# Optimization experiments

Hardware: AMD Instinct MI355X
Metric: run time of the kernel (lower is better)

Reference implementation:

```python
import jax, jax.numpy as jnp
import numpy as np

NUM_HEADS = 12
DIM = 768
HEAD_DIM = DIM // NUM_HEADS
NUM_BUCKETS = 32
MAX_DISTANCE = 128
ELEV_SCALE = 1000.0


def _bucket_positions(relative_position):
    # Faithful port of RelativePositionBias2D._bucket_positions (torch .long() truncates;
    # values passed through the large branch are non-negative so astype(int32) matches).
    nb = NUM_BUCKETS // 2  # 16
    n = -relative_position
    ret = (n < 0).astype(jnp.int32) * nb
    n = jnp.abs(n)
    max_exact = nb // 2  # 8
    is_small = n < max_exact
    n_safe = jnp.maximum(n, 1).astype(jnp.float32)  # avoid log(0); masked by is_small
    val_if_large = max_exact + (
        jnp.log(n_safe / max_exact) / np.float32(np.log(MAX_DISTANCE / max_exact)) * (nb - max_exact)
    ).astype(jnp.int32)
    val_if_large = jnp.minimum(val_if_large, nb - 1)
    return ret + jnp.where(is_small, n, val_if_large)


def _bucket_idx(coords_2d):
    # coords_2d: [B, N, 2] in [0,1] -> integer grid coords
    coords_int = (coords_2d * MAX_DISTANCE).astype(jnp.int32)
    rel_x = coords_int[:, :, None, 0] - coords_int[:, None, :, 0]  # [B,N,N]
    rel_y = coords_int[:, :, None, 1] - coords_int[:, None, :, 1]
    bx = _bucket_positions(rel_x)
    by = _bucket_positions(rel_y)
    return bx * NUM_BUCKETS + by  # [B,N,N] int32 in [0, 1024)


def setup_inputs() -> dict:
    key = jax.random.key(0)
    ks = jax.random.split(key, 8)
    B, N, D = 4, 1024, DIM
    x = jax.random.normal(ks[0], (B, N, D), dtype=jnp.float32)
    coords_2d = jax.random.uniform(ks[1], (B, N, 2), dtype=jnp.float32)
    elevation_patches = jax.random.normal(ks[2], (B, N), dtype=jnp.float32) * 2000.0  # meters
    qkv_w = jax.random.normal(ks[3], (3 * D, D), dtype=jnp.float32) * 0.02
    qkv_b = jnp.zeros((3 * D,), dtype=jnp.float32)
    proj_w = jax.random.normal(ks[4], (D, D), dtype=jnp.float32) * 0.02
    proj_b = jnp.zeros((D,), dtype=jnp.float32)
    bias_table = jax.random.normal(ks[5], (NUM_BUCKETS * NUM_BUCKETS, NUM_HEADS), dtype=jnp.float32) * 0.02
    alpha = jnp.full((1,), 2.0, dtype=jnp.float32)
    return {"x": x, "coords_2d": coords_2d, "elevation_patches": elevation_patches,
            "qkv_w": qkv_w, "qkv_b": qkv_b, "proj_w": proj_w, "proj_b": proj_b,
            "bias_table": bias_table, "alpha": alpha}


def reference(x, coords_2d, elevation_patches, qkv_w, qkv_b, proj_w, proj_b, bias_table, alpha):
    B, N, D = x.shape
    H, hd = NUM_HEADS, HEAD_DIM
    scale = hd ** -0.5

    qkv = x @ qkv_w.T + qkv_b  # [B,N,3D]
    qkv = qkv.reshape(B, N, 3, H, hd)
    q = qkv[:, :, 0].transpose(0, 2, 1, 3)  # [B,H,N,hd]
    k = qkv[:, :, 1].transpose(0, 2, 1, 3)
    v = qkv[:, :, 2].transpose(0, 2, 1, 3)

    attn = jnp.einsum('bhnd,bhmd->bhnm', q * scale, k)  # [B,H,N,N]

    # relative position bias: gather from table, [B,N,N,H] -> [B,H,N,N]
    idx = _bucket_idx(coords_2d)
    rel_bias = bias_table[idx].transpose(0, 3, 1, 2)
    attn = attn + rel_bias

    # elevation bias: [B,N,N], broadcast over heads
    elev_diff = (elevation_patches[:, None, :] - elevation_patches[:, :, None]) / ELEV_SCALE
    elev_bias = jnp.clip(-alpha[0] * jax.nn.relu(elev_diff), -10.0, 0.0)
    attn = attn + elev_bias[:, None, :, :]

    attn = jax.nn.softmax(attn.astype(jnp.float32), axis=-1).astype(q.dtype)

    out = jnp.einsum('bhnm,bhmd->bhnd', attn, v)  # [B,H,N,hd]
    out = out.transpose(0, 2, 1, 3).reshape(B, N, D)
    return out @ proj_w.T + proj_b
```

## Files before the change

### kernel.cpp

```cpp
#include <hip/hip_runtime.h>
#include <hip/hip_bf16.h>
#include <math.h>

#define NH 12
#define HD 64
#define NSEQ 1024
#define DMODEL 768
#define LOG2E 1.44269504f

typedef unsigned short ushort_t;
typedef float f32x4 __attribute__((ext_vector_type(4)));
typedef short bf16x8 __attribute__((ext_vector_type(8)));

__device__ __forceinline__ ushort_t f2bf(float f) {
    unsigned int u = __float_as_uint(f);
    u += 0x7FFFu + ((u >> 16) & 1u);
    return (ushort_t)(u >> 16);
}

__device__ __forceinline__ unsigned pk2(float x, float y) {
    __hip_bfloat162 t = __float22bfloat162_rn(make_float2(x, y));
    union { __hip_bfloat162 b; unsigned u; } c; c.b = t;
    return c.u;
}

__device__ __forceinline__ void gl_lds16(const ushort_t* g, ushort_t* l) {
    __builtin_amdgcn_global_load_lds(
        (const __attribute__((address_space(1))) unsigned int*)g,
        (__attribute__((address_space(3))) unsigned int*)l, 16, 0, 0);
}

#define XB_N   3145728u
#define WQB_N  1769472u
#define PWB_N  589824u
#define CVT_BLOCKS 2688

__device__ __forceinline__ int bucketf(int rel) {
    const int n = -rel;
    const int u = (n < 0) ? 16 : 0;
    const int a = n < 0 ? -n : n;
    if (a < 8) return u + a;
    int v = 8 + (int)(log2f((float)a * 0.125f) * 2.0f + 1e-4f);
    if (v > 15) v = 15;
    return u + v;
}

__global__ __launch_bounds__(256) void prep_kernel(
    const float* __restrict__ x, const float* __restrict__ w1,
    const float* __restrict__ w2, ushort_t* __restrict__ dst,
    const float* __restrict__ coords, const float* __restrict__ elev,
    const float* __restrict__ alpha_p, unsigned* __restrict__ pack)
{
    const int t = threadIdx.x;
    if (blockIdx.x < CVT_BLOCKS) {
        const unsigned i = blockIdx.x * 256 + t;
        const unsigned n0 = XB_N / 8, n1 = n0 + WQB_N / 8, n2 = n1 + PWB_N / 8;
        if (i >= n2) return;
        const float* src; unsigned off;
        if (i < n0)      { src = x;  off = i; }
        else if (i < n1) { src = w1; off = i - n0; }
        else             { src = w2; off = i - n1; }
        const float4 a = ((const float4*)src)[off * 2];
        const float4 b = ((const float4*)src)[off * 2 + 1];
        uint4 pk;
        pk.x = pk2(a.x, a.y); pk.y = pk2(a.z, a.w);
        pk.z = pk2(b.x, b.y); pk.w = pk2(b.z, b.w);
        ((uint4*)dst)[i] = pk;
    } else {
        const int blk = blockIdx.x - CVT_BLOCKS;
        const int b = blk >> 10, i = blk & 1023;
        const float alpha = alpha_p[0];
        const float2 ci = *(const float2*)&coords[(size_t)(b * NSEQ + i) * 2];
        const int cxi = (int)(ci.x * 128.0f), cyi = (int)(ci.y * 128.0f);
        const float ei = elev[b * NSEQ + i];
        const int j0 = t * 4;
        const float4 c01 = *(const float4*)&coords[(size_t)(b * NSEQ + j0) * 2];
        const float4 c23 = *(const float4*)&coords[(size_t)(b * NSEQ + j0 + 2) * 2];
        const float4 ej4 = *(const float4*)&elev[b * NSEQ + j0];
        const float cjx[4] = {c01.x, c01.z, c23.x, c23.z};
        const float cjy[4] = {c01.y, c01.w, c23.y, c23.w};
        const float ejv[4] = {ej4.x, ej4.y, ej4.z, ej4.w};
        unsigned r[4];
        #pragma unroll
        for (int k = 0; k < 4; ++k) {
            const int bx = bucketf(cxi - (int)(cjx[k] * 128.0f));
            const int by = bucketf(cyi - (int)(cjy[k] * 128.0f));
            const int idx = (bx << 5) + by;
            const float ed = (ejv[k] - ei) * 1e-3f;
            const float eb = fmaxf(-alpha * fmaxf(ed, 0.0f), -10.0f) * LOG2E;
            r[k] = ((unsigned)f2bf(eb) << 16) | (unsigned)idx;
        }
        uint4 o; o.x = r[0]; o.y = r[1]; o.z = r[2]; o.w = r[3];
        *(uint4*)&pack[((size_t)b << 20) + (size_t)i * NSEQ + j0] = o;
    }
}

__global__ __launch_bounds__(256) void qkv_gemm(
    const ushort_t* __restrict__ A, const ushort_t* __restrict__ B,
    const float* __restrict__ bias,
    ushort_t* __restrict__ Qb, ushort_t* __restrict__ Kb, ushort_t* __restrict__ Vtb)
{
    __shared__ __align__(16) ushort_t SM[6144];
    ushort_t* Asb = SM;
    ushort_t* Bsb = SM + 4096;
    const int t = threadIdx.x;
    const int lane = t & 63, w = t >> 6;
    const int wr = w >> 1, wc = w & 1;
    const int col = lane & 15, quad = lane >> 4;
    const int m0 = blockIdx.y * 128, c0 = blockIdx.x * 64;

    const f32x4 zero = {0.f, 0.f, 0.f, 0.f};
    f32x4 acc[4][2];
    #pragma unroll
    for (int i = 0; i < 4; ++i)
        #pragma unroll
        for (int j = 0; j < 2; ++j) acc[i][j] = zero;

    const int arow = w * 32 + (lane >> 2);
    const int brow = w * 16 + (lane >> 2);
    const int scol = (lane & 3) * 8;
    const ushort_t* Ag = A + (size_t)(m0 + arow) * DMODEL + scol;
    const ushort_t* Bg = B + (size_t)(c0 + brow) * DMODEL + scol;
    ushort_t* Asw = Asb + w * 32 * 32;
    ushort_t* Bsw = Bsb + w * 16 * 32;

    for (int k0 = 0; k0 < DMODEL; k0 += 32) {
        __syncthreads();
        gl_lds16(Ag + k0, Asw);
        gl_lds16(Ag + (size_t)16 * DMODEL + k0, Asw + 16 * 32);
        gl_lds16(Bg + k0, Bsw);
        __syncthreads();
        bf16x8 af[4], bf[2];
        #pragma unroll
        for (int im = 0; im < 4; ++im)
            af[im] = *(const bf16x8*)&Asb[(wr * 64 + im * 16 + col) * 32 + quad * 8];
        #pragma unroll
        for (int jn = 0; jn < 2; ++jn)
            bf[jn] = *(const bf16x8*)&Bsb[(wc * 32 + jn * 16 + col) * 32 + quad * 8];
        #pragma unroll
        for (int im = 0; im < 4; ++im)
            #pragma unroll
            for (int jn = 0; jn < 2; ++jn)
                acc[im][jn] = __builtin_amdgcn_mfma_f32_16x16x32_bf16(af[im], bf[jn], acc[im][jn], 0, 0, 0);
    }

    const int s = c0 / DMODEL;
    const int h = (c0 % DMODEL) >> 6;
    const int b = m0 >> 10;
    const int bh = b * NH + h;
    const int n0 = (m0 & (NSEQ - 1)) + wr * 64;
    const int d0 = (c0 & 63);
    const int cb = c0 + wc * 32;

    __syncthreads();

    if (s < 2) {
        ushort_t* lt = SM + w * 1280;
        ushort_t* dst = (s == 0) ? Qb : Kb;
        const float sc = (s == 0) ? 0.125f * LOG2E : 1.0f;
        float bv[2];
        #pragma unroll
        for (int jn = 0; jn < 2; ++jn) bv[jn] = bias[cb + jn * 16 + col];
        const int row16 = lane >> 2, seg = lane & 3;
        #pragma unroll
        for (int im = 0; im < 4; ++im) {
            #pragma unroll
            for (int jn = 0; jn < 2; ++jn) {
                const f32x4 a = acc[im][jn];
                #pragma unroll
                for (int r = 0; r < 4; ++r)
                    lt[(quad * 4 + r) * 40 + jn * 16 + col] = f2bf((a[r] + bv[jn]) * sc);
            }
            const uint4 u0 = *(const uint4*)&lt[row16 * 40 + seg * 8];
            const size_t gb = ((size_t)bh * NSEQ + n0 + im * 16 + row16) * HD
                            + wc * 32 + seg * 8;
            *(uint4*)&dst[gb] = u0;
        }
    } else {
        #pragma unroll
        for (int im = 0; im < 4; ++im) {
            #pragma unroll
            for (int jn = 0; jn < 2; ++jn) {
                const int d = wc * 32 + jn * 16 + col;
                const float bvv = bias[cb + jn * 16 + col];
                const f32x4 a = acc[im][jn];
                uint2 p;
                p.x = pk2(a[0] + bvv, a[1] + bvv);
                p.y = pk2(a[2] + bvv, a[3] + bvv);
                *(uint2*)&Vtb[((size_t)bh * HD + d) * NSEQ + n0 + im * 16 + quad * 4] = p;
            }
        }
    }
    (void)d0;
}

__global__ __launch_bounds__(256) void attn_mfma(
    const ushort_t* __restrict__ Qb, const ushort_t* __restrict__ Kb,
    const ushort_t* __restrict__ Vtb,
    const unsigned* __restrict__ pack,
    const float* __restrict__ table,
    ushort_t* __restrict__ Ob)
{
    __shared__ __align__(16) ushort_t Ks[2][64 * 72];
    __shared__ __align__(16) ushort_t Vt[2][64 * 72];
    __shared__ __align__(16) ushort_t Ps[64 * 72];
    __shared__ ushort_t tabu[1024];

    const int t = threadIdx.x;
    const int lane = t & 63, w = t >> 6;
    const int col = lane & 15, quad = lane >> 4;
    const int bid = blockIdx.x;
    const int it = bid & 15, bh = bid >> 4;
    const int h = bh % NH, b = bh / NH;
    const int i0 = it * 64;

    for (int i = t; i < 1024; i += 256)
        tabu[i] = f2bf(table[i * NH + h] * LOG2E);

    const ushort_t* Qg = Qb + ((size_t)bh * NSEQ + i0 + w * 16 + col) * HD;
    const bf16x8 aq0 = *(const bf16x8*)(Qg + quad * 8);
    const bf16x8 aq1 = *(const bf16x8*)(Qg + 32 + quad * 8);

    const size_t kvbase = (size_t)bh * NSEQ * HD;
    const unsigned* prow = pack + ((size_t)b << 20)
                         + (size_t)(i0 + w * 16 + col) * NSEQ + quad * 4;

    const int srow = t >> 3, sc8 = (t & 7) * 8;
    const int so0 = srow * 72 + sc8;
    const int so1 = (srow + 32) * 72 + sc8;

    uint4 k0 = *(const uint4*)&Kb[kvbase + (size_t)srow * HD + sc8];
    uint4 k1 = *(const uint4*)&Kb[kvbase + (size_t)(srow + 32) * HD + sc8];
    uint4 v0 = *(const uint4*)&Vtb[kvbase + (size_t)srow * NSEQ + sc8];
    uint4 v1 = *(const uint4*)&Vtb[kvbase + (size_t)(srow + 32) * NSEQ + sc8];
    *(uint4*)&Ks[0][so0] = k0;
    *(uint4*)&Ks[0][so1] = k1;
    *(uint4*)&Vt[0][so0] = v0;
    *(uint4*)&Vt[0][so1] = v1;
    k0 = *(const uint4*)&Kb[kvbase + (size_t)(64 + srow) * HD + sc8];
    k1 = *(const uint4*)&Kb[kvbase + (size_t)(64 + srow + 32) * HD + sc8];
    v0 = *(const uint4*)&Vtb[kvbase + (size_t)srow * NSEQ + 64 + sc8];
    v1 = *(const uint4*)&Vtb[kvbase + (size_t)(srow + 32) * NSEQ + 64 + sc8];

    const f32x4 zero = {0.f, 0.f, 0.f, 0.f};
    f32x4 o_acc[4];
    #pragma unroll
    for (int i = 0; i < 4; ++i) o_acc[i] = zero;
    float l_l = 0.f;

    #pragma unroll 2
    for (int jt = 0; jt < 16; ++jt) {
        __syncthreads();
        const int cur = jt & 1;
        const int j0 = jt * 64;

        if (jt < 15) {
            *(uint4*)&Ks[cur ^ 1][so0] = k0;
            *(uint4*)&Ks[cur ^ 1][so1] = k1;
            *(uint4*)&Vt[cur ^ 1][so0] = v0;
            *(uint4*)&Vt[cur ^ 1][so1] = v1;
        }
        if (jt < 14) {
            const int j2 = (jt + 2) * 64;
            k0 = *(const uint4*)&Kb[kvbase + (size_t)(j2 + srow) * HD + sc8];
            k1 = *(const uint4*)&Kb[kvbase + (size_t)(j2 + srow + 32) * HD + sc8];
            v0 = *(const uint4*)&Vtb[kvbase + (size_t)srow * NSEQ + j2 + sc8];
            v1 = *(const uint4*)&Vtb[kvbase + (size_t)(srow + 32) * NSEQ + j2 + sc8];
        }
        uint4 pk4[4];
        #pragma unroll
        for (int jb = 0; jb < 4; ++jb)
            pk4[jb] = *(const uint4*)(prow + j0 + jb * 16);

        f32x4 sacc[4];
        #pragma unroll
        for (int jb = 0; jb < 4; ++jb) {
            sacc[jb] = zero;
            const bf16x8 kb0 = *(const bf16x8*)&Ks[cur][(jb * 16 + col) * 72 + quad * 8];
            const bf16x8 kb1 = *(const bf16x8*)&Ks[cur][(jb * 16 + col) * 72 + 32 + quad * 8];
            sacc[jb] = __builtin_amdgcn_mfma_f32_16x16x32_bf16(kb0, aq0, sacc[jb], 0, 0, 0);
            sacc[jb] = __builtin_amdgcn_mfma_f32_16x16x32_bf16(kb1, aq1, sacc[jb], 0, 0, 0);
        }

        float rbeb[4][4];
        #pragma unroll
        for (int jb = 0; jb < 4; ++jb) {
            const uint4 pkv = pk4[jb];
            rbeb[jb][0] = __uint_as_float((unsigned)tabu[pkv.x & 1023u] << 16) + __uint_as_float(pkv.x & 0xFFFF0000u);
            rbeb[jb][1] = __uint_as_float((unsigned)tabu[pkv.y & 1023u] << 16) + __uint_as_float(pkv.y & 0xFFFF0000u);
            rbeb[jb][2] = __uint_as_float((unsigned)tabu[pkv.z & 1023u] << 16) + __uint_as_float(pkv.z & 0xFFFF0000u);
            rbeb[jb][3] = __uint_as_float((unsigned)tabu[pkv.w & 1023u] << 16) + __uint_as_float(pkv.w & 0xFFFF0000u);
        }

        float psum = 0.f;
        #pragma unroll
        for (int jb = 0; jb < 4; ++jb) {
            const float p0 = exp2f(sacc[jb][0] + rbeb[jb][0]);
            const float p1 = exp2f(sacc[jb][1] + rbeb[jb][1]);
            const float p2 = exp2f(sacc[jb][2] + rbeb[jb][2]);
            const float p3 = exp2f(sacc[jb][3] + rbeb[jb][3]);
            psum += (p0 + p1) + (p2 + p3);
            uint2 st;
            st.x = pk2(p0, p1);
            st.y = pk2(p2, p3);
            *(uint2*)&Ps[(w * 16 + col) * 72 + jb * 16 + quad * 4] = st;
        }
        l_l += psum;

        const bf16x8 ap0 = *(const bf16x8*)&Ps[(w * 16 + col) * 72 + quad * 8];
        const bf16x8 ap1 = *(const bf16x8*)&Ps[(w * 16 + col) * 72 + 32 + quad * 8];
        #pragma unroll
        for (int db = 0; db < 4; ++db) {
            const bf16x8 vv0 = *(const bf16x8*)&Vt[cur][(db * 16 + col) * 72 + quad * 8];
            const bf16x8 vv1 = *(const bf16x8*)&Vt[cur][(db * 16 + col) * 72 + 32 + quad * 8];
            o_acc[db] = __builtin_amdgcn_mfma_f32_16x16x32_bf16(ap0, vv0, o_acc[db], 0, 0, 0);
            o_acc[db] = __builtin_amdgcn_mfma_f32_16x16x32_bf16(ap1, vv1, o_acc[db], 0, 0, 0);
        }
    }

    float l = l_l;
    l += __shfl_xor(l, 16);
    l += __shfl_xor(l, 32);
    #pragma unroll
    for (int r = 0; r < 4; ++r) {
        const float lr = __shfl(l, w * 16 + quad * 4 + r);
        const float inv = 1.f / lr;
        const int ri = w * 16 + quad * 4 + r;
        const size_t base = ((size_t)(b * NSEQ) + i0 + ri) * DMODEL + h * HD;
        #pragma unroll
        for (int db = 0; db < 4; ++db)
            Ob[base + db * 16 + col] = f2bf(o_acc[db][r] * inv);
    }
}

__global__ __launch_bounds__(256) void proj_gemm(
    const ushort_t* __restrict__ A, const ushort_t* __restrict__ B,
    const float* __restrict__ bias, float* __restrict__ out)
{
    __shared__ __align__(16) ushort_t As[64 * 32];
    __shared__ __align__(16) ushort_t Bs[64 * 32];
    const int t = threadIdx.x;
    const int lane = t & 63, w = t >> 6;
    const int wr = w >> 1, wc = w & 1;
    const int col = lane & 15, quad = lane >> 4;
    const int m0 = blockIdx.y * 64, c0 = blockIdx.x * 64;

    const f32x4 zero = {0.f, 0.f, 0.f, 0.f};
    f32x4 acc[2][2];
    #pragma unroll
    for (int i = 0; i < 2; ++i)
        #pragma unroll
        for (int j = 0; j < 2; ++j) acc[i][j] = zero;

    const int srow = w * 16 + (lane >> 2);
    const int scol = (lane & 3) * 8;
    const ushort_t* Ag = A + (size_t)(m0 + srow) * DMODEL + scol;
    const ushort_t* Bg = B + (size_t)(c0 + srow) * DMODEL + scol;
    ushort_t* Asw = &As[w * 16 * 32];
    ushort_t* Bsw = &Bs[w * 16 * 32];

    for (int k0 = 0; k0 < DMODEL; k0 += 32) {
        __syncthreads();
        gl_lds16(Ag + k0, Asw);
        gl_lds16(Bg + k0, Bsw);
        __syncthreads();
        bf16x8 af[2], bf[2];
        #pragma unroll
        for (int im = 0; im < 2; ++im)
            af[im] = *(const bf16x8*)&As[(wr * 32 + im * 16 + col) * 32 + quad * 8];
        #pragma unroll
        for (int jn = 0; jn < 2; ++jn)
            bf[jn] = *(const bf16x8*)&Bs[(wc * 32 + jn * 16 + col) * 32 + quad * 8];
        #pragma unroll
        for (int im = 0; im < 2; ++im)
            #pragma unroll
            for (int jn = 0; jn < 2; ++jn)
                acc[im][jn] = __builtin_amdgcn_mfma_f32_16x16x32_bf16(af[im], bf[jn], acc[im][jn], 0, 0, 0);
    }

    #pragma unroll
    for (int im = 0; im < 2; ++im) {
        #pragma unroll
        for (int jn = 0; jn < 2; ++jn) {
            const int c = c0 + wc * 32 + jn * 16 + col;
            const float bv = bias[c];
            #pragma unroll
            for (int r = 0; r < 4; ++r) {
                const int m = m0 + wr * 32 + im * 16 + quad * 4 + r;
                out[(size_t)m * DMODEL + c] = acc[im][jn][r] + bv;
            }
        }
    }
}

extern "C" void kernel_launch(void* const* d_in, const int* in_sizes, int n_in,
                              void* d_out, int out_size, void* d_ws, size_t ws_size,
                              hipStream_t stream) {
    const float* x       = (const float*)d_in[0];
    const float* coords  = (const float*)d_in[1];
    const float* elev    = (const float*)d_in[2];
    const float* qkv_w   = (const float*)d_in[3];
    const float* qkv_b   = (const float*)d_in[4];
    const float* proj_w  = (const float*)d_in[5];
    const float* proj_b  = (const float*)d_in[6];
    const float* btable  = (const float*)d_in[7];
    const float* alpha   = (const float*)d_in[8];
    float* out = (float*)d_out;

    ushort_t* wsu = (ushort_t*)d_ws;
    ushort_t* xb  = wsu;
    ushort_t* wqb = wsu + 3145728;
    ushort_t* pwb = wsu + 4915200;
    ushort_t* Qb  = wsu + 5505024;
    ushort_t* Kb  = wsu + 8650752;
    ushort_t* Vtb = wsu + 11796480;
    ushort_t* Ob  = wsu + 14942208;
    unsigned* pck = (unsigned*)(wsu + 18087936);

    prep_kernel<<<CVT_BLOCKS + 4096, 256, 0, stream>>>(
        x, qkv_w, proj_w, wsu, coords, elev, alpha, pck);
    qkv_gemm<<<dim3(36, 32), 256, 0, stream>>>(xb, wqb, qkv_b, Qb, Kb, Vtb);
    attn_mfma<<<768, 256, 0, stream>>>(Qb, Kb, Vtb, pck, btable, Ob);
    proj_gemm<<<dim3(12, 64), 256, 0, stream>>>(Ob, pwb, proj_b, out);
}
```

Measured before the change: 186.4 us.

## Software-pipeline bias pack loads and remap block order in attention kernel

Prefetches the packed relative-position/elevation bias words two tiles ahead and computes each next tile's bias lookups while the P·V MFMAs run, so the global-load latency and LDS table lookups overlap with matrix work. It also remaps blockIdx so consecutive blocks fall on different (batch, head) groups, which should spread work across XCDs and improve K/V cache locality. The MFMA sections are wrapped in s_setprio to favour matrix issue. In exchange it raises register pressure (extra bias and pack arrays) and adds a barrier before the first table use.

After: 185.9 us. Within noise of the previous version (-0.2%).

```diff
diff --git a/kernel.cpp b/kernel.cpp
--- a/kernel.cpp
+++ b/kernel.cpp
@@ -194,6 +194,9 @@
     (void)d0;
 }
 
+#define RBIAS(u) (__uint_as_float((unsigned)tabu[(u) & 1023u] << 16) \
+                + __uint_as_float((u) & 0xFFFF0000u))
+
 __global__ __launch_bounds__(256) void attn_mfma(
     const ushort_t* __restrict__ Qb, const ushort_t* __restrict__ Kb,
     const ushort_t* __restrict__ Vtb,
@@ -209,7 +212,7 @@
     const int t = threadIdx.x;
     const int lane = t & 63, w = t >> 6;
     const int col = lane & 15, quad = lane >> 4;
-    const int bid = blockIdx.x;
+    const int bid = (blockIdx.x & 7) * 96 + (blockIdx.x >> 3);
     const int it = bid & 15, bh = bid >> 4;
     const int h = bh % NH, b = bh / NH;
     const int i0 = it * 64;
@@ -242,6 +245,26 @@
     v0 = *(const uint4*)&Vtb[kvbase + (size_t)srow * NSEQ + 64 + sc8];
     v1 = *(const uint4*)&Vtb[kvbase + (size_t)(srow + 32) * NSEQ + 64 + sc8];
 
+    uint4 pk4g[4], pk4l[4];
+    #pragma unroll
+    for (int jb = 0; jb < 4; ++jb)
+        pk4g[jb] = *(const uint4*)(prow + jb * 16);
+
+    __syncthreads();
+
+    float rbc[4][4], rbn[4][4];
+    #pragma unroll
+    for (int jb = 0; jb < 4; ++jb) {
+        const uint4 pkv = pk4g[jb];
+        rbc[jb][0] = RBIAS(pkv.x);
+        rbc[jb][1] = RBIAS(pkv.y);
+        rbc[jb][2] = RBIAS(pkv.z);
+        rbc[jb][3] = RBIAS(pkv.w);
+    }
+    #pragma unroll
+    for (int jb = 0; jb < 4; ++jb)
+        pk4g[jb] = *(const uint4*)(prow + 64 + jb * 16);
+
     const f32x4 zero = {0.f, 0.f, 0.f, 0.f};
     f32x4 o_acc[4];
     #pragma unroll
@@ -252,7 +275,6 @@
     for (int jt = 0; jt < 16; ++jt) {
         __syncthreads();
         const int cur = jt & 1;
-        const int j0 = jt * 64;
 
         if (jt < 15) {
             *(uint4*)&Ks[cur ^ 1][so0] = k0;
@@ -266,13 +288,13 @@
             k1 = *(const uint4*)&Kb[kvbase + (size_t)(j2 + srow + 32) * HD + sc8];
             v0 = *(const uint4*)&Vtb[kvbase + (size_t)srow * NSEQ + j2 + sc8];
             v1 = *(const uint4*)&Vtb[kvbase + (size_t)(srow + 32) * NSEQ + j2 + sc8];
-        }
-        uint4 pk4[4];
-        #pragma unroll
-        for (int jb = 0; jb < 4; ++jb)
-            pk4[jb] = *(const uint4*)(prow + j0 + jb * 16);
+            #pragma unroll
+            for (int jb = 0; jb < 4; ++jb)
+                pk4l[jb] = *(const uint4*)(prow + j2 + jb * 16);
+        }
 
         f32x4 sacc[4];
+        __builtin_amdgcn_s_setprio(1);
         #pragma unroll
         for (int jb = 0; jb < 4; ++jb) {
             sacc[jb] = zero;
@@ -281,24 +303,15 @@
             sacc[jb] = __builtin_amdgcn_mfma_f32_16x16x32_bf16(kb0, aq0, sacc[jb], 0, 0, 0);
             sacc[jb] = __builtin_amdgcn_mfma_f32_16x16x32_bf16(kb1, aq1, sacc[jb], 0, 0, 0);
         }
-
-        float rbeb[4][4];
+        __builtin_amdgcn_s_setprio(0);
+
+        float psum = 0.f;
         #pragma unroll
         for (int jb = 0; jb < 4; ++jb) {
-            const uint4 pkv = pk4[jb];
-            rbeb[jb][0] = __uint_as_float((unsigned)tabu[pkv.x & 1023u] << 16) + __uint_as_float(pkv.x & 0xFFFF0000u);
-            rbeb[jb][1] = __uint_as_float((unsigned)tabu[pkv.y & 1023u] << 16) + __uint_as_float(pkv.y & 0xFFFF0000u);
-            rbeb[jb][2] = __uint_as_float((unsigned)tabu[pkv.z & 1023u] << 16) + __uint_as_float(pkv.z & 0xFFFF0000u);
-            rbeb[jb][3] = __uint_as_float((unsigned)tabu[pkv.w & 1023u] << 16) + __uint_as_float(pkv.w & 0xFFFF0000u);
-        }
-
-        float psum = 0.f;
-        #pragma unroll
-        for (int jb = 0; jb < 4; ++jb) {
-            const float p0 = exp2f(sacc[jb][0] + rbeb[jb][0]);
-            const float p1 = exp2f(sacc[jb][1] + rbeb[jb][1]);
-            const float p2 = exp2f(sacc[jb][2] + rbeb[jb][2]);
-            const float p3 = exp2f(sacc[jb][3] + rbeb[jb][3]);
+            const float p0 = exp2f(sacc[jb][0] + rbc[jb][0]);
+            const float p1 = exp2f(sacc[jb][1] + rbc[jb][1]);
+            const float p2 = exp2f(sacc[jb][2] + rbc[jb][2]);
+            const float p3 = exp2f(sacc[jb][3] + rbc[jb][3]);
             psum += (p0 + p1) + (p2 + p3);
             uint2 st;
             st.x = pk2(p0, p1);
@@ -309,12 +322,30 @@
 
         const bf16x8 ap0 = *(const bf16x8*)&Ps[(w * 16 + col) * 72 + quad * 8];
         const bf16x8 ap1 = *(const bf16x8*)&Ps[(w * 16 + col) * 72 + 32 + quad * 8];
+        __builtin_amdgcn_s_setprio(1);
         #pragma unroll
         for (int db = 0; db < 4; ++db) {
             const bf16x8 vv0 = *(const bf16x8*)&Vt[cur][(db * 16 + col) * 72 + quad * 8];
             const bf16x8 vv1 = *(const bf16x8*)&Vt[cur][(db * 16 + col) * 72 + 32 + quad * 8];
             o_acc[db] = __builtin_amdgcn_mfma_f32_16x16x32_bf16(ap0, vv0, o_acc[db], 0, 0, 0);
             o_acc[db] = __builtin_amdgcn_mfma_f32_16x16x32_bf16(ap1, vv1, o_acc[db], 0, 0, 0);
+            if (jt < 15) {
+                const uint4 pkv = pk4g[db];
+                rbn[db][0] = RBIAS(pkv.x);
+                rbn[db][1] = RBIAS(pkv.y);
+                rbn[db][2] = RBIAS(pkv.z);
+                rbn[db][3] = RBIAS(pkv.w);
+            }
+        }
+        __builtin_amdgcn_s_setprio(0);
+
+        #pragma unroll
+        for (int jb = 0; jb < 4; ++jb) {
+            pk4g[jb] = pk4l[jb];
+            rbc[jb][0] = rbn[jb][0];
+            rbc[jb][1] = rbn[jb][1];
+            rbc[jb][2] = rbn[jb][2];
+            rbc[jb][3] = rbn[jb][3];
         }
     }
 
```
